# Kernel optimization log

Hardware: AMD Instinct MI355X
Metric: run time of the kernel (lower is better)

Reference implementation:

```python
import jax, jax.numpy as jnp
import numpy as np

N = 100000
E = 1600000
D = 128
L = 4
G = 64
EPS = 1e-5


def _bn(x, g, b, m, v):
    # BatchNorm1d in eval mode: normalize with running stats
    return (x - m) * jax.lax.rsqrt(v + EPS) * g + b


def setup_inputs() -> dict:
    key = jax.random.key(0)
    ks = jax.random.split(key, 32)
    x = jax.random.normal(ks[0], (N, 11), jnp.float32)
    pos = jax.random.normal(ks[1], (N, 3), jnp.float32)
    edge_index = jax.random.randint(ks[2], (2, E), 0, N)
    edge_attr = jax.random.normal(ks[3], (E, 4), jnp.float32)
    batch = jnp.sort(jax.random.randint(ks[4], (N,), 0, G))
    s = 0.05
    lin_in_w = jax.random.normal(ks[5], (14, D), jnp.float32) * s
    lin_in_b = jnp.zeros((D,), jnp.float32)
    msg_w1 = jax.random.normal(ks[6], (L, 2 * D + 4, D), jnp.float32) * s
    msg_b1 = jnp.zeros((L, D), jnp.float32)
    msg_bn_g = jnp.ones((L, D), jnp.float32)
    msg_bn_b = jnp.zeros((L, D), jnp.float32)
    msg_bn_m = jax.random.normal(ks[7], (L, D), jnp.float32) * s
    msg_bn_v = jax.random.uniform(ks[8], (L, D), jnp.float32, 0.5, 1.5)
    msg_w2 = jax.random.normal(ks[9], (L, D, D), jnp.float32) * s
    msg_b2 = jnp.zeros((L, D), jnp.float32)
    upd_w1 = jax.random.normal(ks[10], (L, 2 * D, D), jnp.float32) * s
    upd_b1 = jnp.zeros((L, D), jnp.float32)
    upd_bn_g = jnp.ones((L, D), jnp.float32)
    upd_bn_b = jnp.zeros((L, D), jnp.float32)
    upd_bn_m = jax.random.normal(ks[11], (L, D), jnp.float32) * s
    upd_bn_v = jax.random.uniform(ks[12], (L, D), jnp.float32, 0.5, 1.5)
    upd_w2 = jax.random.normal(ks[13], (L, D, D), jnp.float32) * s
    upd_b2 = jnp.zeros((L, D), jnp.float32)
    pred_w = jax.random.normal(ks[14], (D, 1), jnp.float32) * s
    pred_b = jnp.zeros((1,), jnp.float32)
    return dict(x=x, pos=pos, edge_index=edge_index, edge_attr=edge_attr, batch=batch,
                lin_in_w=lin_in_w, lin_in_b=lin_in_b,
                msg_w1=msg_w1, msg_b1=msg_b1, msg_bn_g=msg_bn_g, msg_bn_b=msg_bn_b,
                msg_bn_m=msg_bn_m, msg_bn_v=msg_bn_v, msg_w2=msg_w2, msg_b2=msg_b2,
                upd_w1=upd_w1, upd_b1=upd_b1, upd_bn_g=upd_bn_g, upd_bn_b=upd_bn_b,
                upd_bn_m=upd_bn_m, upd_bn_v=upd_bn_v, upd_w2=upd_w2, upd_b2=upd_b2,
                pred_w=pred_w, pred_b=pred_b)


def reference(x, pos, edge_index, edge_attr, batch,
              lin_in_w, lin_in_b,
              msg_w1, msg_b1, msg_bn_g, msg_bn_b, msg_bn_m, msg_bn_v, msg_w2, msg_b2,
              upd_w1, upd_b1, upd_bn_g, upd_bn_b, upd_bn_m, upd_bn_v, upd_w2, upd_b2,
              pred_w, pred_b):
    src = edge_index[0]  # j (source)
    dst = edge_index[1]  # i (target, aggregation index)
    h = jnp.concatenate([x, pos], axis=-1) @ lin_in_w + lin_in_b  # [N, D]
    for l in range(L):
        # message: cat(h_i, h_j, edge_attr) -> Linear -> ReLU -> BN -> Linear -> ReLU
        m = jnp.concatenate([h[dst], h[src], edge_attr], axis=-1)  # [E, 2D+4]
        m = jax.nn.relu(m @ msg_w1[l] + msg_b1[l])
        m = _bn(m, msg_bn_g[l], msg_bn_b[l], msg_bn_m[l], msg_bn_v[l])
        m = jax.nn.relu(m @ msg_w2[l] + msg_b2[l])  # [E, D]
        # aggregate: scatter-add on target nodes
        aggr = jax.ops.segment_sum(m, dst, num_segments=N)  # [N, D]
        # update: cat(h, aggr) -> Linear -> ReLU -> BN -> Linear -> ReLU
        u = jnp.concatenate([h, aggr], axis=-1)
        u = jax.nn.relu(u @ upd_w1[l] + upd_b1[l])
        u = _bn(u, upd_bn_g[l], upd_bn_b[l], upd_bn_m[l], upd_bn_v[l])
        u = jax.nn.relu(u @ upd_w2[l] + upd_b2[l])
        h = h + u  # residual
    # global mean pool over graphs
    sums = jax.ops.segment_sum(h, batch, num_segments=G)
    cnts = jax.ops.segment_sum(jnp.ones((N,), h.dtype), batch, num_segments=G)
    h_graph = sums / jnp.maximum(cnts, 1.0)[:, None]
    out = h_graph @ pred_w + pred_b  # [G, 1]
    return out.reshape(-1)
```

## Files before the change

### kernel.cpp

```cpp
#include <hip/hip_runtime.h>
#include <hip/hip_bf16.h>


#define EPSBN 1e-5f
#define TS 136
#define AS 264

typedef __bf16 bf16x8 __attribute__((ext_vector_type(8)));
typedef float floatx4 __attribute__((ext_vector_type(4)));
typedef float f32x2 __attribute__((ext_vector_type(2)));

#if __has_builtin(__builtin_elementwise_fma)
#define VFMA(a, b, c) __builtin_elementwise_fma((a), (b), (c))
#else
#define VFMA(a, b, c) ((a) * (b) + (c))
#endif
#if __has_builtin(__builtin_elementwise_max)
#define VMAX(a, b) __builtin_elementwise_max((a), (b))
#else
static __device__ __forceinline__ f32x2 VMAX(f32x2 a, f32x2 b) {
  f32x2 r; r.x = fmaxf(a.x, b.x); r.y = fmaxf(a.y, b.y); return r;
}
#endif

static __device__ __forceinline__ unsigned short f2b(float f) {
  union { float f; unsigned u; } v; v.f = f;
  unsigned u = v.u;
  return (unsigned short)((u + 0x7fffu + ((u >> 16) & 1u)) >> 16);
}
static __device__ __forceinline__ unsigned pk2(float lo, float hi) {
  union { __hip_bfloat162 h; unsigned u; } v;
  v.h = __float22bfloat162_rn(make_float2(lo, hi));
  return v.u;
}
static __device__ __forceinline__ float ubits(unsigned u) {
  union { unsigned u; float f; } v; v.u = u; return v.f;
}
static __device__ __forceinline__ f32x2 mk2(float a, float b) {
  f32x2 r; r.x = a; r.y = b; return r;
}
static __device__ __forceinline__ f32x2 sp2(float a) { return mk2(a, a); }
static __device__ __forceinline__ f32x2 up2(unsigned u) {
  return mk2(ubits(u << 16), ubits(u & 0xffff0000u));
}

__global__ __launch_bounds__(128) void fold_kernel(
    const float* __restrict__ mw2, const float* __restrict__ mb2,
    const float* __restrict__ mg, const float* __restrict__ mb,
    const float* __restrict__ mm, const float* __restrict__ mv,
    const float* __restrict__ uw2, const float* __restrict__ ub2,
    const float* __restrict__ ug, const float* __restrict__ ub,
    const float* __restrict__ um, const float* __restrict__ uv,
    unsigned short* __restrict__ mW2fT, float* __restrict__ mB2f,
    unsigned short* __restrict__ uW2fT, float* __restrict__ uB2f) {
  int l = blockIdx.x & 3;
  bool isu = blockIdx.x >= 4;
  const float* W2 = (isu ? uw2 : mw2) + (size_t)l * 128 * 128;
  const float* b2 = (isu ? ub2 : mb2) + l * 128;
  const float* gg = (isu ? ug : mg) + l * 128;
  const float* bb = (isu ? ub : mb) + l * 128;
  const float* mn = (isu ? um : mm) + l * 128;
  const float* vr = (isu ? uv : mv) + l * 128;
  unsigned short* WfT = (isu ? uW2fT : mW2fT) + (size_t)l * 128 * 128;
  float* Bf = (isu ? uB2f : mB2f) + l * 128;
  __shared__ float a[128], c[128];
  int d = threadIdx.x;
  float ad = gg[d] * rsqrtf(vr[d] + EPSBN);
  a[d] = ad;
  c[d] = bb[d] - mn[d] * ad;
  __syncthreads();
  float acc = b2[d];
  for (int k = 0; k < 128; ++k) {
    float w = W2[k * 128 + d];
    WfT[(size_t)d * 128 + k] = f2b(a[k] * w);
    acc = fmaf(c[k], w, acc);
  }
  Bf[d] = acc;
}

__global__ __launch_bounds__(256) void transp_kernel(
    const float* __restrict__ mw1, const float* __restrict__ uw1,
    unsigned short* __restrict__ W1abT, unsigned short* __restrict__ U1T) {
  int l = blockIdx.x & 3;
  bool isu = blockIdx.x >= 4;
  int tid = threadIdx.x;
  if (!isu) {
    const float* W = mw1 + (size_t)l * 260 * 128;
    unsigned short* T = W1abT + (size_t)l * 256 * 128;
    for (int i = tid; i < 256 * 128; i += 256) {
      int n = i >> 7, k = i & 127;
      float v = (n < 128) ? W[(size_t)k * 128 + n] : W[(size_t)(128 + k) * 128 + (n - 128)];
      T[i] = f2b(v);
    }
  } else {
    const float* W = uw1 + (size_t)l * 256 * 128;
    unsigned short* T = U1T + (size_t)l * 128 * 256;
    for (int i = tid; i < 128 * 256; i += 256) {
      int n = i >> 8, k = i & 255;
      T[i] = f2b(W[(size_t)k * 128 + n]);
    }
  }
}

__global__ __launch_bounds__(256) void lin_in_kernel(
    const float* __restrict__ x, const float* __restrict__ pos,
    const float* __restrict__ W, const float* __restrict__ b,
    float* __restrict__ h, int Nn) {
  int gi = blockIdx.x * 256 + threadIdx.x;
  if (gi >= Nn * 128) return;
  int n = gi >> 7, d = gi & 127;
  float acc = b[d];
#pragma unroll
  for (int j = 0; j < 11; ++j) acc = fmaf(x[(size_t)n * 11 + j], W[j * 128 + d], acc);
#pragma unroll
  for (int j = 0; j < 3; ++j) acc = fmaf(pos[(size_t)n * 3 + j], W[(11 + j) * 128 + d], acc);
  h[gi] = acc;
}

__global__ __launch_bounds__(256) void hist_kernel(const int* __restrict__ dst, int* __restrict__ count, int Ee) {
  int i = blockIdx.x * 256 + threadIdx.x;
  if (i < Ee) atomicAdd(&count[dst[i]], 1);
}

__global__ __launch_bounds__(1024) void scan1_kernel(
    const int* __restrict__ count, int* __restrict__ cursor, int* __restrict__ bsum, int n) {
  __shared__ int buf[1024];
  int i = blockIdx.x * 1024 + threadIdx.x;
  int v = (i < n) ? count[i] : 0;
  buf[threadIdx.x] = v;
  __syncthreads();
  for (int off = 1; off < 1024; off <<= 1) {
    int t = (threadIdx.x >= off) ? buf[threadIdx.x - off] : 0;
    __syncthreads();
    buf[threadIdx.x] += t;
    __syncthreads();
  }
  if (i < n) cursor[i] = buf[threadIdx.x] - v;
  if (threadIdx.x == 1023) bsum[blockIdx.x] = buf[1023];
}
__global__ __launch_bounds__(1024) void scan2_kernel(int* __restrict__ bsum, int nb) {
  __shared__ int buf[1024];
  int v = (threadIdx.x < nb) ? bsum[threadIdx.x] : 0;
  buf[threadIdx.x] = v;
  __syncthreads();
  for (int off = 1; off < 1024; off <<= 1) {
    int t = (threadIdx.x >= off) ? buf[threadIdx.x - off] : 0;
    __syncthreads();
    buf[threadIdx.x] += t;
    __syncthreads();
  }
  if (threadIdx.x < nb) bsum[threadIdx.x] = buf[threadIdx.x] - v;
}
__global__ __launch_bounds__(1024) void scan3_kernel(
    int* __restrict__ cursor, const int* __restrict__ bsum, int n) {
  int i = blockIdx.x * 1024 + threadIdx.x;
  if (i < n) cursor[i] += bsum[blockIdx.x];
}

__global__ __launch_bounds__(256) void scatter_kernel(
    const int* __restrict__ src, const int* __restrict__ dst, const float* __restrict__ ea,
    int* __restrict__ cursor, int* __restrict__ dst_s, int* __restrict__ src_s,
    float* __restrict__ ea_s, int Ee) {
  int e = blockIdx.x * 256 + threadIdx.x;
  if (e >= Ee) return;
  int dn = dst[e];
  int pos = atomicAdd(&cursor[dn], 1);
  dst_s[pos] = dn;
  src_s[pos] = src[e];
  *(float4*)(ea_s + (size_t)pos * 4) = *(const float4*)(ea + (size_t)e * 4);
}

__global__ __launch_bounds__(256) void mask_kernel(
    const int* __restrict__ dst_s, unsigned long long* __restrict__ masks, int Ee, int nt) {
  int tile = blockIdx.x * 4 + (threadIdx.x >> 6);
  int lane = threadIdx.x & 63;
  if (tile >= nt) return;
  int e = tile * 64 + lane;
  bool start;
  if (e >= Ee || lane == 0) start = true;
  else start = (dst_s[e] != dst_s[e - 1]);
  unsigned long long m = __ballot(start);
  if (lane == 0) masks[tile] = m;
}

__global__ __launch_bounds__(256) void pq_kernel(
    const float* __restrict__ h, const unsigned short* __restrict__ W1abT,
    unsigned short* __restrict__ P, unsigned short* __restrict__ Q, int Nn) {
  __shared__ unsigned short hs[64 * TS];
  const int tid = threadIdx.x;
  const int row0 = blockIdx.x * 64;
#pragma unroll
  for (int i = 0; i < 8; ++i) {
    int idx = tid + i * 256;
    int r = idx >> 5, c4 = (idx & 31) << 2;
    float4 v = make_float4(0.f, 0.f, 0.f, 0.f);
    if (row0 + r < Nn) v = *(const float4*)(h + (size_t)(row0 + r) * 128 + c4);
    *(uint2*)&hs[r * TS + c4] = make_uint2(pk2(v.x, v.y), pk2(v.z, v.w));
  }
  __syncthreads();
  const int lane = tid & 63, wv = tid >> 6;
  const int m16 = lane & 15, quad = lane >> 4;
  floatx4 acc[4][4];
#pragma unroll
  for (int mt = 0; mt < 4; ++mt)
#pragma unroll
    for (int nt = 0; nt < 4; ++nt) acc[mt][nt] = (floatx4)(0.0f);
  const __bf16* WT = (const __bf16*)W1abT;
  const __bf16* TlB = (const __bf16*)hs;
#pragma unroll
  for (int kb = 0; kb < 4; ++kb) {
    bf16x8 a[4], w[4];
#pragma unroll
    for (int mt = 0; mt < 4; ++mt)
      a[mt] = *(const bf16x8*)(TlB + (16 * mt + m16) * TS + kb * 32 + quad * 8);
#pragma unroll
    for (int nt = 0; nt < 4; ++nt)
      w[nt] = *(const bf16x8*)(WT + (size_t)(64 * wv + 16 * nt + m16) * 128 + kb * 32 + quad * 8);
#pragma unroll
    for (int mt = 0; mt < 4; ++mt)
#pragma unroll
      for (int nt = 0; nt < 4; ++nt)
        acc[mt][nt] = __builtin_amdgcn_mfma_f32_16x16x32_bf16(w[nt], a[mt], acc[mt][nt], 0, 0, 0);
  }
#pragma unroll
  for (int mt = 0; mt < 4; ++mt) {
    int row = row0 + 16 * mt + m16;
    if (row >= Nn) continue;
#pragma unroll
    for (int nt = 0; nt < 4; ++nt) {
      int n0 = 64 * wv + 16 * nt + 4 * quad;
      floatx4 A = acc[mt][nt];
      uint2 o = make_uint2(pk2(A[0], A[1]), pk2(A[2], A[3]));
      if (n0 < 128) *(uint2*)(P + (size_t)row * 128 + n0) = o;
      else *(uint2*)(Q + (size_t)row * 128 + (n0 - 128)) = o;
    }
  }
}

static __device__ __forceinline__ void gather_q(
    const unsigned short* __restrict__ Q, const int* __restrict__ ssrcBase,
    int rw, int c0, uint4* qv) {
#pragma unroll
  for (int p = 0; p < 4; ++p) {
    int sna = ssrcBase[16 * p + rw];
    qv[p] = *(const uint4*)(Q + (size_t)sna * 128 + c0);
  }
}

static __device__ __forceinline__ void build_T(
    unsigned short* __restrict__ TlBuf,
    const unsigned short* __restrict__ P, const uint4* qv,
    const int* __restrict__ sdstBase, const float* __restrict__ seaBase,
    const f32x2 (*__restrict__ wc2)[4], const f32x2* __restrict__ b1v, int rw, int c0) {
  uint4 pv[4];
#pragma unroll
  for (int p = 0; p < 4; ++p) {
    int dn = sdstBase[16 * p + rw];
    int dna = dn < 0 ? 0 : dn;
    pv[p] = *(const uint4*)(P + (size_t)dna * 128 + c0);
  }
#pragma unroll
  for (int p = 0; p < 4; ++p) {
    int row = 16 * p + rw;
    int dn = sdstBase[row];
    uint4 out = make_uint4(0u, 0u, 0u, 0u);
    if (dn >= 0) {
      float e0 = seaBase[row * 4 + 0], e1 = seaBase[row * 4 + 1];
      float e2 = seaBase[row * 4 + 2], e3 = seaBase[row * 4 + 3];
      unsigned pu[4] = {pv[p].x, pv[p].y, pv[p].z, pv[p].w};
      unsigned qu[4] = {qv[p].x, qv[p].y, qv[p].z, qv[p].w};
      unsigned ou[4];
#pragma unroll
      for (int g = 0; g < 4; ++g) {
        f32x2 t = up2(pu[g]) + up2(qu[g]) + b1v[g];
        t = VFMA(sp2(e0), wc2[0][g], t);
        t = VFMA(sp2(e1), wc2[1][g], t);
        t = VFMA(sp2(e2), wc2[2][g], t);
        t = VFMA(sp2(e3), wc2[3][g], t);
        t = VMAX(t, sp2(0.f));
        ou[g] = pk2(t.x, t.y);
      }
      out = make_uint4(ou[0], ou[1], ou[2], ou[3]);
    }
    *(uint4*)&TlBuf[row * TS + c0] = out;
  }
}

static __device__ __forceinline__ void mfma_B(
    const unsigned short* __restrict__ TlBuf, const __bf16* __restrict__ WT,
    int m16, int quad, int wv, floatx4 acc[4][2]) {
#pragma unroll
  for (int mt = 0; mt < 4; ++mt) { acc[mt][0] = (floatx4)(0.0f); acc[mt][1] = (floatx4)(0.0f); }
  const __bf16* TlB = (const __bf16*)TlBuf;
#pragma unroll
  for (int kb = 0; kb < 4; ++kb) {
    bf16x8 w0 = *(const bf16x8*)(WT + (size_t)(32 * wv + m16) * 128 + kb * 32 + quad * 8);
    bf16x8 w1 = *(const bf16x8*)(WT + (size_t)(32 * wv + 16 + m16) * 128 + kb * 32 + quad * 8);
    bf16x8 a[4];
#pragma unroll
    for (int mt = 0; mt < 4; ++mt)
      a[mt] = *(const bf16x8*)(TlB + (16 * mt + m16) * TS + kb * 32 + quad * 8);
#pragma unroll
    for (int mt = 0; mt < 4; ++mt) {
      acc[mt][0] = __builtin_amdgcn_mfma_f32_16x16x32_bf16(w0, a[mt], acc[mt][0], 0, 0, 0);
      acc[mt][1] = __builtin_amdgcn_mfma_f32_16x16x32_bf16(w1, a[mt], acc[mt][1], 0, 0, 0);
    }
  }
}

static __device__ __forceinline__ void epi_m(
    unsigned short* __restrict__ TlBuf, floatx4 acc[4][2],
    const float* __restrict__ B2f, int m16, int quad, int wv) {
  int n0 = 32 * wv + 4 * quad;
  float4 b0 = *(const float4*)(B2f + n0);
  float4 b1q = *(const float4*)(B2f + n0 + 16);
  f32x2 bz0 = mk2(b0.x, b0.y), bz1 = mk2(b0.z, b0.w);
  f32x2 bz2 = mk2(b1q.x, b1q.y), bz3 = mk2(b1q.z, b1q.w);
#pragma unroll
  for (int mt = 0; mt < 4; ++mt) {
    int row = 16 * mt + m16;
    floatx4 A0 = acc[mt][0], A1 = acc[mt][1];
    f32x2 t0 = VMAX(mk2(A0[0], A0[1]) + bz0, sp2(0.f));
    f32x2 t1 = VMAX(mk2(A0[2], A0[3]) + bz1, sp2(0.f));
    f32x2 t2 = VMAX(mk2(A1[0], A1[1]) + bz2, sp2(0.f));
    f32x2 t3 = VMAX(mk2(A1[2], A1[3]) + bz3, sp2(0.f));
    *(uint2*)&TlBuf[row * TS + n0] = make_uint2(pk2(t0.x, t0.y), pk2(t1.x, t1.y));
    *(uint2*)&TlBuf[row * TS + n0 + 16] = make_uint2(pk2(t2.x, t2.y), pk2(t3.x, t3.y));
  }
}

static __device__ __forceinline__ void seg_reduce(
    const unsigned short* __restrict__ TlBuf, const int* __restrict__ sdstBase,
    unsigned long long mask, float* __restrict__ aggr, int tid) {
  const int c4 = (tid & 15) << 2;
  const int st = tid >> 4;
  const int dfirst = sdstBase[0], dlast = sdstBase[63];
  for (int s = st; s < 64; s += 16) {
    if (!(mask & (1ull << s))) continue;
    int dn = sdstBase[s];
    if (dn < 0) continue;
    int end;
    if (s >= 63) end = 64;
    else {
      unsigned long long m2 = mask >> (s + 1);
      end = m2 ? (s + 1 + (int)__builtin_ctzll(m2)) : 64;
    }
    f32x2 a0 = sp2(0.f), a1 = sp2(0.f), a2 = sp2(0.f), a3 = sp2(0.f);
    for (int e = s; e < end; ++e) {
      uint2 v1 = *(const uint2*)&TlBuf[e * TS + c4];
      uint2 v2 = *(const uint2*)&TlBuf[e * TS + 64 + c4];
      a0 += up2(v1.x); a1 += up2(v1.y);
      a2 += up2(v2.x); a3 += up2(v2.y);
    }
    float* ap = aggr + (size_t)dn * 128 + c4;
    if (dn == dfirst || dn == dlast) {
      atomicAdd(ap + 0, a0.x); atomicAdd(ap + 1, a0.y);
      atomicAdd(ap + 2, a1.x); atomicAdd(ap + 3, a1.y);
      atomicAdd(ap + 64, a2.x); atomicAdd(ap + 65, a2.y);
      atomicAdd(ap + 66, a3.x); atomicAdd(ap + 67, a3.y);
    } else {
      *(float4*)ap = make_float4(a0.x, a0.y, a1.x, a1.y);
      *(float4*)(ap + 64) = make_float4(a2.x, a2.y, a3.x, a3.y);
    }
  }
}

__global__ __launch_bounds__(256, 4) void edge_kernel(
    const unsigned short* __restrict__ P, const unsigned short* __restrict__ Q,
    const float* __restrict__ ea_s, const int* __restrict__ dst_s, const int* __restrict__ src_s,
    const unsigned long long* __restrict__ masks,
    const float* __restrict__ W1c, const float* __restrict__ b1,
    const unsigned short* __restrict__ W2fT, const float* __restrict__ B2f,
    float* __restrict__ aggr, int Ee, int nT) {
  __shared__ unsigned short Tl[2][64 * TS];
  __shared__ float sea[128 * 4];
  __shared__ int sdst[128], ssrc[128];
  const int tid = threadIdx.x;
  int b = blockIdx.x;
  const int nB = gridDim.x;
  const int per = nB >> 3;
  if (b < (per << 3)) b = (b & 7) * per + (b >> 3);
  const int t0 = b * 2, t1 = t0 + 1;
  const int e0 = t0 * 64;
  const bool has1 = (t1 < nT);
  const unsigned long long mask0 = masks[t0];
  const unsigned long long mask1 = has1 ? masks[t1] : 0ull;
  if (tid < 128) {
    int e = e0 + tid;
    bool ok = e < Ee;
    sdst[tid] = ok ? dst_s[e] : -1;
    ssrc[tid] = ok ? src_s[e] : 0;
    float4 ev = ok ? *(const float4*)(ea_s + (size_t)e * 4) : make_float4(0.f, 0.f, 0.f, 0.f);
    *(float4*)&sea[tid * 4] = ev;
  }
  const int lane = tid & 63, wv = tid >> 6;
  const int m16 = lane & 15, quad = lane >> 4;
  const int rw = tid >> 4, c0 = (tid & 15) << 3;

  f32x2 wc2[4][4], b1v[4];
#pragma unroll
  for (int r = 0; r < 4; ++r) {
    float4 u = *(const float4*)(W1c + r * 128 + c0);
    float4 v = *(const float4*)(W1c + r * 128 + c0 + 4);
    wc2[r][0] = mk2(u.x, u.y); wc2[r][1] = mk2(u.z, u.w);
    wc2[r][2] = mk2(v.x, v.y); wc2[r][3] = mk2(v.z, v.w);
  }
  {
    float4 u = *(const float4*)(b1 + c0);
    float4 v = *(const float4*)(b1 + c0 + 4);
    b1v[0] = mk2(u.x, u.y); b1v[1] = mk2(u.z, u.w);
    b1v[2] = mk2(v.x, v.y); b1v[3] = mk2(v.z, v.w);
  }
  const __bf16* WT = (const __bf16*)W2fT;
  __syncthreads();

  uint4 qv[4], qv1[4];
  gather_q(Q, ssrc, rw, c0, qv);
  build_T(Tl[0], P, qv, sdst, sea, wc2, b1v, rw, c0);
  if (has1) gather_q(Q, ssrc + 64, rw, c0, qv1);
  __syncthreads();

  floatx4 acc[4][2];
  mfma_B(Tl[0], WT, m16, quad, wv, acc);
  if (has1) build_T(Tl[1], P, qv1, sdst + 64, sea + 256, wc2, b1v, rw, c0);
  __syncthreads();

  epi_m(Tl[0], acc, B2f, m16, quad, wv);
  __syncthreads();

  if (has1) mfma_B(Tl[1], WT, m16, quad, wv, acc);
  seg_reduce(Tl[0], sdst, mask0, aggr, tid);
  if (has1) {
    __syncthreads();
    epi_m(Tl[1], acc, B2f, m16, quad, wv);
    __syncthreads();
    seg_reduce(Tl[1], sdst + 64, mask1, aggr, tid);
  }
}

__global__ __launch_bounds__(256) void upd_kernel(
    float* __restrict__ h, const float* __restrict__ aggr,
    const unsigned short* __restrict__ U1T, const float* __restrict__ ub1,
    const unsigned short* __restrict__ uW2fT, const float* __restrict__ uB2f, int Nn,
    const unsigned short* __restrict__ W1abT_next,
    unsigned short* __restrict__ P, unsigned short* __restrict__ Q) {
  __shared__ unsigned short as_[64 * AS];
  const int tid = threadIdx.x;
  const int row0 = blockIdx.x * 64;
#pragma unroll
  for (int i = 0; i < 8; ++i) {
    int idx = tid + i * 256;
    int r = idx >> 5, c4 = (idx & 31) << 2;
    float4 v = make_float4(0.f, 0.f, 0.f, 0.f);
    if (row0 + r < Nn) v = *(const float4*)(h + (size_t)(row0 + r) * 128 + c4);
    *(uint2*)&as_[r * AS + c4] = make_uint2(pk2(v.x, v.y), pk2(v.z, v.w));
  }
#pragma unroll
  for (int i = 0; i < 8; ++i) {
    int idx = tid + i * 256;
    int r = idx >> 5, c4 = (idx & 31) << 2;
    float4 v = make_float4(0.f, 0.f, 0.f, 0.f);
    if (row0 + r < Nn) v = *(const float4*)(aggr + (size_t)(row0 + r) * 128 + c4);
    *(uint2*)&as_[r * AS + 128 + c4] = make_uint2(pk2(v.x, v.y), pk2(v.z, v.w));
  }
  __syncthreads();
  const int lane = tid & 63, wv = tid >> 6;
  const int m16 = lane & 15, quad = lane >> 4;
  const __bf16* asB = (const __bf16*)as_;
  unsigned short* u1s = as_;
  {
    floatx4 acc[4][2];
#pragma unroll
    for (int mt = 0; mt < 4; ++mt) { acc[mt][0] = (floatx4)(0.0f); acc[mt][1] = (floatx4)(0.0f); }
    const __bf16* WT = (const __bf16*)U1T;
#pragma unroll
    for (int kb = 0; kb < 8; ++kb) {
      bf16x8 w0 = *(const bf16x8*)(WT + (size_t)(32 * wv + m16) * 256 + kb * 32 + quad * 8);
      bf16x8 w1 = *(const bf16x8*)(WT + (size_t)(32 * wv + 16 + m16) * 256 + kb * 32 + quad * 8);
      bf16x8 a[4];
#pragma unroll
      for (int mt = 0; mt < 4; ++mt)
        a[mt] = *(const bf16x8*)(asB + (16 * mt + m16) * AS + kb * 32 + quad * 8);
#pragma unroll
      for (int mt = 0; mt < 4; ++mt) {
        acc[mt][0] = __builtin_amdgcn_mfma_f32_16x16x32_bf16(w0, a[mt], acc[mt][0], 0, 0, 0);
        acc[mt][1] = __builtin_amdgcn_mfma_f32_16x16x32_bf16(w1, a[mt], acc[mt][1], 0, 0, 0);
      }
    }
    __syncthreads();
    int n0 = 32 * wv + 4 * quad;
    float4 bv0 = *(const float4*)(ub1 + n0);
    float4 bv1 = *(const float4*)(ub1 + n0 + 16);
#pragma unroll
    for (int mt = 0; mt < 4; ++mt) {
      int row = 16 * mt + m16;
      floatx4 A0 = acc[mt][0], A1 = acc[mt][1];
      *(uint2*)&u1s[row * TS + n0] =
          make_uint2(pk2(fmaxf(A0[0] + bv0.x, 0.f), fmaxf(A0[1] + bv0.y, 0.f)),
                     pk2(fmaxf(A0[2] + bv0.z, 0.f), fmaxf(A0[3] + bv0.w, 0.f)));
      *(uint2*)&u1s[row * TS + n0 + 16] =
          make_uint2(pk2(fmaxf(A1[0] + bv1.x, 0.f), fmaxf(A1[1] + bv1.y, 0.f)),
                     pk2(fmaxf(A1[2] + bv1.z, 0.f), fmaxf(A1[3] + bv1.w, 0.f)));
    }
  }
  __syncthreads();
  {
    floatx4 acc[4][2];
#pragma unroll
    for (int mt = 0; mt < 4; ++mt) { acc[mt][0] = (floatx4)(0.0f); acc[mt][1] = (floatx4)(0.0f); }
    const __bf16* WT = (const __bf16*)uW2fT;
    const __bf16* u1B = (const __bf16*)u1s;
#pragma unroll
    for (int kb = 0; kb < 4; ++kb) {
      bf16x8 w0 = *(const bf16x8*)(WT + (size_t)(32 * wv + m16) * 128 + kb * 32 + quad * 8);
      bf16x8 w1 = *(const bf16x8*)(WT + (size_t)(32 * wv + 16 + m16) * 128 + kb * 32 + quad * 8);
      bf16x8 a[4];
#pragma unroll
      for (int mt = 0; mt < 4; ++mt)
        a[mt] = *(const bf16x8*)(u1B + (16 * mt + m16) * TS + kb * 32 + quad * 8);
#pragma unroll
      for (int mt = 0; mt < 4; ++mt) {
        acc[mt][0] = __builtin_amdgcn_mfma_f32_16x16x32_bf16(w0, a[mt], acc[mt][0], 0, 0, 0);
        acc[mt][1] = __builtin_amdgcn_mfma_f32_16x16x32_bf16(w1, a[mt], acc[mt][1], 0, 0, 0);
      }
    }
    __syncthreads();
    int n0 = 32 * wv + 4 * quad;
    float4 bv0 = *(const float4*)(uB2f + n0);
    float4 bv1 = *(const float4*)(uB2f + n0 + 16);
#pragma unroll
    for (int mt = 0; mt < 4; ++mt) {
      int rloc = 16 * mt + m16;
      int row = row0 + rloc;
      floatx4 A0 = acc[mt][0], A1 = acc[mt][1];
      if (row < Nn) {
        float* hp0 = h + (size_t)row * 128 + n0;
        float4 hv0 = *(float4*)hp0;
        float4 o0 = make_float4(hv0.x + fmaxf(A0[0] + bv0.x, 0.f), hv0.y + fmaxf(A0[1] + bv0.y, 0.f),
                                hv0.z + fmaxf(A0[2] + bv0.z, 0.f), hv0.w + fmaxf(A0[3] + bv0.w, 0.f));
        *(float4*)hp0 = o0;
        float* hp1 = hp0 + 16;
        float4 hv1 = *(float4*)hp1;
        float4 o1 = make_float4(hv1.x + fmaxf(A1[0] + bv1.x, 0.f), hv1.y + fmaxf(A1[1] + bv1.y, 0.f),
                                hv1.z + fmaxf(A1[2] + bv1.z, 0.f), hv1.w + fmaxf(A1[3] + bv1.w, 0.f));
        *(float4*)hp1 = o1;
        if (W1abT_next) {
          *(uint2*)&u1s[rloc * TS + n0] = make_uint2(pk2(o0.x, o0.y), pk2(o0.z, o0.w));
          *(uint2*)&u1s[rloc * TS + n0 + 16] = make_uint2(pk2(o1.x, o1.y), pk2(o1.z, o1.w));
        }
      } else if (W1abT_next) {
        *(uint2*)&u1s[rloc * TS + n0] = make_uint2(0u, 0u);
        *(uint2*)&u1s[rloc * TS + n0 + 16] = make_uint2(0u, 0u);
      }
    }
  }
  if (W1abT_next) {
    __syncthreads();
    floatx4 pacc[4][4];
#pragma unroll
    for (int mt = 0; mt < 4; ++mt)
#pragma unroll
      for (int nt = 0; nt < 4; ++nt) pacc[mt][nt] = (floatx4)(0.0f);
    const __bf16* WT = (const __bf16*)W1abT_next;
    const __bf16* hB = (const __bf16*)u1s;
#pragma unroll
    for (int kb = 0; kb < 4; ++kb) {
      bf16x8 a[4], w[4];
#pragma unroll
      for (int mt = 0; mt < 4; ++mt)
        a[mt] = *(const bf16x8*)(hB + (16 * mt + m16) * TS + kb * 32 + quad * 8);
#pragma unroll
      for (int nt = 0; nt < 4; ++nt)
        w[nt] = *(const bf16x8*)(WT + (size_t)(64 * wv + 16 * nt + m16) * 128 + kb * 32 + quad * 8);
#pragma unroll
      for (int mt = 0; mt < 4; ++mt)
#pragma unroll
        for (int nt = 0; nt < 4; ++nt)
          pacc[mt][nt] = __builtin_amdgcn_mfma_f32_16x16x32_bf16(w[nt], a[mt], pacc[mt][nt], 0, 0, 0);
    }
#pragma unroll
    for (int mt = 0; mt < 4; ++mt) {
      int row = row0 + 16 * mt + m16;
      if (row >= Nn) continue;
#pragma unroll
      for (int nt = 0; nt < 4; ++nt) {
        int n0 = 64 * wv + 16 * nt + 4 * quad;
        floatx4 A = pacc[mt][nt];
        uint2 o = make_uint2(pk2(A[0], A[1]), pk2(A[2], A[3]));
        if (n0 < 128) *(uint2*)(P + (size_t)row * 128 + n0) = o;
        else *(uint2*)(Q + (size_t)row * 128 + (n0 - 128)) = o;
      }
    }
  }
}

__global__ __launch_bounds__(128) void pool_sum_kernel(
    const float* __restrict__ h, const int* __restrict__ batch,
    float* __restrict__ sums, int* __restrict__ gcnt, int Nn) {
  int n0 = blockIdx.x * 256;
  if (n0 >= Nn) return;
  int nend = min(n0 + 256, Nn);
  int d = threadIdx.x;
  int gcur = batch[n0];
  float run = 0.f;
  int cnt = 0;
  for (int n = n0; n < nend; ++n) {
    int g = batch[n];
    if (g != gcur) {
      atomicAdd(&sums[(size_t)gcur * 128 + d], run);
      if (d == 0) atomicAdd(&gcnt[gcur], cnt);
      run = 0.f; cnt = 0; gcur = g;
    }
    run += h[(size_t)n * 128 + d];
    cnt += 1;
  }
  atomicAdd(&sums[(size_t)gcur * 128 + d], run);
  if (d == 0) atomicAdd(&gcnt[gcur], cnt);
}

__global__ __launch_bounds__(128) void pred_kernel(
    const float* __restrict__ sums, const int* __restrict__ gcnt,
    const float* __restrict__ pw, const float* __restrict__ pb, float* __restrict__ out) {
  __shared__ float red[2];
  int g = blockIdx.x, d = threadIdx.x;
  float c = fmaxf((float)gcnt[g], 1.f);
  float v = (sums[(size_t)g * 128 + d] / c) * pw[d];
  for (int o = 32; o > 0; o >>= 1) v += __shfl_down(v, o, 64);
  if ((d & 63) == 0) red[d >> 6] = v;
  __syncthreads();
  if (d == 0) out[g] = red[0] + red[1] + pb[0];
}

extern "C" void kernel_launch(void* const* d_in, const int* in_sizes, int n_in,
                              void* d_out, int out_size, void* d_ws, size_t ws_size,
                              hipStream_t stream) {
  const float* x = (const float*)d_in[0];
  const float* pos = (const float*)d_in[1];
  const int* ei = (const int*)d_in[2];
  const float* ea = (const float*)d_in[3];
  const int* batch = (const int*)d_in[4];
  const float* lin_w = (const float*)d_in[5];
  const float* lin_b = (const float*)d_in[6];
  const float* mw1 = (const float*)d_in[7];
  const float* mb1 = (const float*)d_in[8];
  const float* mg = (const float*)d_in[9];
  const float* mbb = (const float*)d_in[10];
  const float* mm = (const float*)d_in[11];
  const float* mv = (const float*)d_in[12];
  const float* mw2 = (const float*)d_in[13];
  const float* mb2 = (const float*)d_in[14];
  const float* uw1 = (const float*)d_in[15];
  const float* ub1 = (const float*)d_in[16];
  const float* ug = (const float*)d_in[17];
  const float* ubb = (const float*)d_in[18];
  const float* um = (const float*)d_in[19];
  const float* uv = (const float*)d_in[20];
  const float* uw2 = (const float*)d_in[21];
  const float* ub2 = (const float*)d_in[22];
  const float* pw = (const float*)d_in[23];
  const float* pb = (const float*)d_in[24];
  float* out = (float*)d_out;

  const int Nn = in_sizes[0] / 11;
  const int Ee = in_sizes[3] / 4;
  const int* srcp = ei;
  const int* dstp = ei + Ee;

  char* wsb = (char*)d_ws;
  size_t off = 0;
  auto alloc = [&](size_t bytes) -> void* {
    void* p = wsb + off;
    off = (off + bytes + 255) & ~(size_t)255;
    return p;
  };
  float* h = (float*)alloc((size_t)Nn * 128 * 4);
  unsigned short* Pb = (unsigned short*)alloc((size_t)Nn * 128 * 2);
  unsigned short* Qb = (unsigned short*)alloc((size_t)Nn * 128 * 2);
  float* aggr = (float*)alloc((size_t)Nn * 128 * 4);
  int* dst_s = (int*)alloc((size_t)Ee * 4);
  int* src_s = (int*)alloc((size_t)Ee * 4);
  float* ea_s = (float*)alloc((size_t)Ee * 16);
  int* count = (int*)alloc((size_t)Nn * 4);
  int* cursor = (int*)alloc((size_t)Nn * 4);
  int* bsum = (int*)alloc((size_t)1024 * 4);
  const int nTiles = (Ee + 63) / 64;
  unsigned long long* masks = (unsigned long long*)alloc((size_t)nTiles * 8);
  unsigned short* mW2fT = (unsigned short*)alloc((size_t)4 * 128 * 128 * 2);
  unsigned short* uW2fT = (unsigned short*)alloc((size_t)4 * 128 * 128 * 2);
  unsigned short* W1abT = (unsigned short*)alloc((size_t)4 * 256 * 128 * 2);
  unsigned short* U1T = (unsigned short*)alloc((size_t)4 * 128 * 256 * 2);
  float* mB2f = (float*)alloc((size_t)4 * 128 * 4);
  float* uB2f = (float*)alloc((size_t)4 * 128 * 4);
  float* sums = (float*)alloc((size_t)out_size * 128 * 4);
  int* gcnt = (int*)alloc((size_t)out_size * 4);
  (void)ws_size; (void)n_in;

  fold_kernel<<<8, 128, 0, stream>>>(mw2, mb2, mg, mbb, mm, mv,
                                     uw2, ub2, ug, ubb, um, uv,
                                     mW2fT, mB2f, uW2fT, uB2f);
  transp_kernel<<<8, 256, 0, stream>>>(mw1, uw1, W1abT, U1T);
  lin_in_kernel<<<(Nn * 128 + 255) / 256, 256, 0, stream>>>(x, pos, lin_w, lin_b, h, Nn);

  hipMemsetAsync(count, 0, (size_t)Nn * 4, stream);
  hist_kernel<<<(Ee + 255) / 256, 256, 0, stream>>>(dstp, count, Ee);
  const int NB = (Nn + 1023) / 1024;
  scan1_kernel<<<NB, 1024, 0, stream>>>(count, cursor, bsum, Nn);
  scan2_kernel<<<1, 1024, 0, stream>>>(bsum, NB);
  scan3_kernel<<<NB, 1024, 0, stream>>>(cursor, bsum, Nn);
  scatter_kernel<<<(Ee + 255) / 256, 256, 0, stream>>>(srcp, dstp, ea, cursor,
                                                       dst_s, src_s, ea_s, Ee);
  mask_kernel<<<(nTiles + 3) / 4, 256, 0, stream>>>(dst_s, masks, Ee, nTiles);

  const int gN = (Nn + 63) / 64;
  pq_kernel<<<gN, 256, 0, stream>>>(h, W1abT, Pb, Qb, Nn);
  for (int l = 0; l < 4; ++l) {
    hipMemsetAsync(aggr, 0, (size_t)Nn * 128 * 4, stream);
    edge_kernel<<<(nTiles + 1) / 2, 256, 0, stream>>>(
        Pb, Qb, ea_s, dst_s, src_s, masks,
        mw1 + (size_t)l * 260 * 128 + 256 * 128, mb1 + l * 128,
        mW2fT + (size_t)l * 16384, mB2f + l * 128, aggr, Ee, nTiles);
    upd_kernel<<<gN, 256, 0, stream>>>(
        h, aggr, U1T + (size_t)l * 128 * 256, ub1 + l * 128,
        uW2fT + (size_t)l * 16384, uB2f + l * 128, Nn,
        (l < 3) ? (W1abT + (size_t)(l + 1) * 256 * 128) : nullptr, Pb, Qb);
  }

  hipMemsetAsync(sums, 0, (size_t)out_size * 128 * 4, stream);
  hipMemsetAsync(gcnt, 0, (size_t)out_size * 4, stream);
  pool_sum_kernel<<<(Nn + 255) / 256, 128, 0, stream>>>(h, batch, sums, gcnt, Nn);
  pred_kernel<<<out_size, 128, 0, stream>>>(sums, gcnt, pw, pb, out);
}
```

Before: 1.773 ms.

## Process one 64-edge tile per edge block instead of two pipelined tiles

The edge kernel drops its two-tile software pipeline, where one tile's build overlapped the other's MFMA, and handles a single 64-edge tile per block. This halves the shared memory per block and removes the second qv register set, so occupancy can rise to 5 blocks per CU, and the grid doubles to nTiles blocks. The cost is losing the intra-block overlap between gather/build and the matrix multiply, plus paying per-block setup (weight loads, masks) twice as often. Edge-attribute loads are also moved to a separate thread range.

```diff
diff --git a/kernel.cpp b/kernel.cpp
--- a/kernel.cpp
+++ b/kernel.cpp
@@ -365,33 +365,34 @@
   }
 }
 
-__global__ __launch_bounds__(256, 4) void edge_kernel(
+__global__ __launch_bounds__(256, 5) void edge_kernel(
     const unsigned short* __restrict__ P, const unsigned short* __restrict__ Q,
     const float* __restrict__ ea_s, const int* __restrict__ dst_s, const int* __restrict__ src_s,
     const unsigned long long* __restrict__ masks,
     const float* __restrict__ W1c, const float* __restrict__ b1,
     const unsigned short* __restrict__ W2fT, const float* __restrict__ B2f,
     float* __restrict__ aggr, int Ee, int nT) {
-  __shared__ unsigned short Tl[2][64 * TS];
-  __shared__ float sea[128 * 4];
-  __shared__ int sdst[128], ssrc[128];
+  __shared__ unsigned short Tl[64 * TS];
+  __shared__ float sea[64 * 4];
+  __shared__ int sdst[64], ssrc[64];
   const int tid = threadIdx.x;
   int b = blockIdx.x;
   const int nB = gridDim.x;
   const int per = nB >> 3;
   if (b < (per << 3)) b = (b & 7) * per + (b >> 3);
-  const int t0 = b * 2, t1 = t0 + 1;
-  const int e0 = t0 * 64;
-  const bool has1 = (t1 < nT);
-  const unsigned long long mask0 = masks[t0];
-  const unsigned long long mask1 = has1 ? masks[t1] : 0ull;
-  if (tid < 128) {
+  const int e0 = b * 64;
+  const unsigned long long mask0 = masks[b];
+  if (tid < 64) {
     int e = e0 + tid;
     bool ok = e < Ee;
     sdst[tid] = ok ? dst_s[e] : -1;
     ssrc[tid] = ok ? src_s[e] : 0;
-    float4 ev = ok ? *(const float4*)(ea_s + (size_t)e * 4) : make_float4(0.f, 0.f, 0.f, 0.f);
-    *(float4*)&sea[tid * 4] = ev;
+  } else if (tid < 128) {
+    int r = tid - 64;
+    int e = e0 + r;
+    float4 ev = (e < Ee) ? *(const float4*)(ea_s + (size_t)e * 4)
+                         : make_float4(0.f, 0.f, 0.f, 0.f);
+    *(float4*)&sea[r * 4] = ev;
   }
   const int lane = tid & 63, wv = tid >> 6;
   const int m16 = lane & 15, quad = lane >> 4;
@@ -414,28 +415,19 @@
   const __bf16* WT = (const __bf16*)W2fT;
   __syncthreads();
 
-  uint4 qv[4], qv1[4];
+  uint4 qv[4];
   gather_q(Q, ssrc, rw, c0, qv);
-  build_T(Tl[0], P, qv, sdst, sea, wc2, b1v, rw, c0);
-  if (has1) gather_q(Q, ssrc + 64, rw, c0, qv1);
+  build_T(Tl, P, qv, sdst, sea, wc2, b1v, rw, c0);
   __syncthreads();
 
   floatx4 acc[4][2];
-  mfma_B(Tl[0], WT, m16, quad, wv, acc);
-  if (has1) build_T(Tl[1], P, qv1, sdst + 64, sea + 256, wc2, b1v, rw, c0);
-  __syncthreads();
-
-  epi_m(Tl[0], acc, B2f, m16, quad, wv);
-  __syncthreads();
-
-  if (has1) mfma_B(Tl[1], WT, m16, quad, wv, acc);
-  seg_reduce(Tl[0], sdst, mask0, aggr, tid);
-  if (has1) {
-    __syncthreads();
-    epi_m(Tl[1], acc, B2f, m16, quad, wv);
-    __syncthreads();
-    seg_reduce(Tl[1], sdst + 64, mask1, aggr, tid);
-  }
+  mfma_B(Tl, WT, m16, quad, wv, acc);
+  __syncthreads();
+
+  epi_m(Tl, acc, B2f, m16, quad, wv);
+  __syncthreads();
+
+  seg_reduce(Tl, sdst, mask0, aggr, tid);
 }
 
 __global__ __launch_bounds__(256) void upd_kernel(
@@ -715,7 +707,7 @@
   pq_kernel<<<gN, 256, 0, stream>>>(h, W1abT, Pb, Qb, Nn);
   for (int l = 0; l < 4; ++l) {
     hipMemsetAsync(aggr, 0, (size_t)Nn * 128 * 4, stream);
-    edge_kernel<<<(nTiles + 1) / 2, 256, 0, stream>>>(
+    edge_kernel<<<nTiles, 256, 0, stream>>>(
         Pb, Qb, ea_s, dst_s, src_s, masks,
         mw1 + (size_t)l * 260 * 128 + 256 * 128, mb1 + l * 128,
         mW2fT + (size_t)l * 16384, mB2f + l * 128, aggr, Ee, nTiles);
```

Result: faster. 1.658 ms (-6.5%).
